# Kernel optimization log

Measured on AMD Instinct MI355X. Metric: run time of the kernel, lower is better.

## Reference

```python
import jax, jax.numpy as jnp
import numpy as np

B, N, IN, HID, H, OUT = 32, 512, 64, 64, 4, 64
NEG_SLOPE = 0.2
NEG_INF = -1e9


def setup_inputs() -> dict:
    key = jax.random.key(0)
    ks = jax.random.split(key, 10)
    s = 0.1
    return {
        "x": jax.random.normal(ks[0], (B, N, IN), jnp.float32),
        "adj": jax.random.randint(ks[1], (B, N, N), 0, 2, jnp.int32),
        "W1": jax.random.normal(ks[2], (IN, H * HID), jnp.float32) * s,
        "a1_src": jax.random.normal(ks[3], (H, HID), jnp.float32) * s,
        "a1_dst": jax.random.normal(ks[4], (H, HID), jnp.float32) * s,
        "b1": jnp.zeros((H * HID,), jnp.float32),
        "W2": jax.random.normal(ks[5], (H * HID, OUT), jnp.float32) * s,
        "a2_src": jax.random.normal(ks[6], (1, OUT), jnp.float32) * s,
        "a2_dst": jax.random.normal(ks[7], (1, OUT), jnp.float32) * s,
        "b2": jnp.zeros((OUT,), jnp.float32),
    }


def _gat_layer(x, mask, W, a_src, a_dst, b, heads, feat):
    # x: [N, Fin]; mask: [N_dst, N_src] bool (edge src->dst), self-loops included
    h = (x @ W).reshape(N, heads, feat)              # [N, H, F]
    e_src = jnp.einsum('nhf,hf->nh', h, a_src)       # [N, H]
    e_dst = jnp.einsum('nhf,hf->nh', h, a_dst)       # [N, H]
    # scores[d, s, h] = leaky_relu(a_dst.x_d + a_src.x_s)
    scores = jax.nn.leaky_relu(e_dst[:, None, :] + e_src[None, :, :], NEG_SLOPE)
    scores = jnp.where(mask[:, :, None], scores, NEG_INF)
    alpha = jax.nn.softmax(scores, axis=1)           # segment-softmax over src neighbors
    out = jnp.einsum('dsh,shf->dhf', alpha, h)       # aggregate messages
    return out.reshape(N, heads * feat) + b


def reference(x, adj, W1, a1_src, a1_dst, b1, W2, a2_src, a2_dst, b2):
    eye = jnp.eye(N, dtype=bool)

    def one_graph(xi, ai):
        # edge i->j when adj[i, j] != 0 (coo row=src, col=dst); add self-loops
        mask = (ai != 0).T | eye                     # [dst, src]
        h1 = jax.nn.elu(_gat_layer(xi, mask, W1, a1_src, a1_dst, b1, H, HID))
        return _gat_layer(h1, mask, W2, a2_src, a2_dst, b2, 1, OUT)

    return jax.vmap(one_graph)(x, adj)               # [B, N, OUT]
```

## Files before the change

### kernel.cpp

```cpp
#include <hip/hip_runtime.h>
#include <cstddef>

#define NN 512
#define NEG_SLOPE 0.2f

typedef __attribute__((ext_vector_type(8))) short short8;
typedef __attribute__((ext_vector_type(16))) float f32x16;

__device__ __forceinline__ unsigned short f2bf(float v) {
  unsigned u = __float_as_uint(v);
  return (unsigned short)((u + 0x7FFFu + ((u >> 16) & 1u)) >> 16);
}

__global__ __launch_bounds__(256) void k_prep(
    const int* __restrict__ adj, const float* __restrict__ x,
    const float* __restrict__ W1, const float* __restrict__ a1s,
    const float* __restrict__ a1d, const float* __restrict__ W2,
    const float* __restrict__ a2s, const float* __restrict__ a2d,
    unsigned* __restrict__ mask, short8* __restrict__ xA,
    short8* __restrict__ W1B, short8* __restrict__ W2B) {
  int blk = blockIdx.x, t = threadIdx.x;
  if (blk < 512) {
    int b = blk >> 4, w = blk & 15;
    const int* base = adj + (size_t)b * NN * NN + (size_t)w * 32 * NN;
#pragma unroll
    for (int half = 0; half < 2; ++half) {
      int d = t + half * 256;
      unsigned wv = 0;
#pragma unroll
      for (int j = 0; j < 32; ++j) {
        unsigned bit = ((base[(size_t)j * NN + d] != 0) || (w * 32 + j == d)) ? 1u : 0u;
        wv |= bit << j;
      }
      mask[((size_t)b * 16 + w) * NN + d] = wv;
    }
  } else if (blk < 1024) {
    int idx = (blk - 512) * 256 + t;
    int u = idx >> 6, lane = idx & 63;
    int b = u >> 6, mt = (u >> 2) & 15, kt = u & 3;
    int node = mt * 32 + (lane & 31);
    int k0 = kt * 16 + ((lane >> 5) << 3);
    const float* xp = x + ((size_t)b * NN + node) * 64 + k0;
    short8 r;
#pragma unroll
    for (int j = 0; j < 8; ++j) r[j] = (short)f2bf(xp[j]);
    xA[idx] = r;
  } else if (blk < 1033) {
    int idx = (blk - 1024) * 256 + t;
    int unit = idx >> 6, lane = idx & 63;
    int nt = unit >> 2, kt = unit & 3;
    int k0 = kt * 16 + ((lane >> 5) << 3);
    short8 r;
    if (nt < 8) {
      int f = nt * 32 + (lane & 31);
#pragma unroll
      for (int j = 0; j < 8; ++j) r[j] = (short)f2bf(W1[(k0 + j) * 256 + f]);
    } else {
      int c = lane & 31;
#pragma unroll
      for (int j = 0; j < 8; ++j) r[j] = 0;
      if (c < 8) {
        int h = c & 3;
        const float* av = ((c < 4) ? a1s : a1d) + h * 64;
#pragma unroll
        for (int j = 0; j < 8; ++j) {
          float s = 0.f;
          for (int f2 = 0; f2 < 64; ++f2)
            s += W1[(k0 + j) * 256 + h * 64 + f2] * av[f2];
          r[j] = (short)f2bf(s);
        }
      }
    }
    W1B[idx] = r;
  } else {
    int idx = (blk - 1033) * 256 + t;
    int unit = idx >> 6, lane = idx & 63;
    int nt = unit >> 4, kt = unit & 15;
    int k0 = kt * 16 + ((lane >> 5) << 3);
    short8 r;
    if (nt < 2) {
      int f = nt * 32 + (lane & 31);
#pragma unroll
      for (int j = 0; j < 8; ++j) r[j] = (short)f2bf(W2[(k0 + j) * 64 + f]);
    } else {
      int c = lane & 31;
#pragma unroll
      for (int j = 0; j < 8; ++j) r[j] = 0;
      if (c < 2) {
        const float* av = (c == 0) ? a2s : a2d;
#pragma unroll
        for (int j = 0; j < 8; ++j) {
          float s = 0.f;
          for (int f2 = 0; f2 < 64; ++f2) s += W2[(k0 + j) * 64 + f2] * av[f2];
          r[j] = (short)f2bf(s);
        }
      }
    }
    W2B[idx] = r;
  }
}

__global__ __launch_bounds__(64) void k_gemm1(const short8* __restrict__ xA,
                                              const short8* __restrict__ W1B,
                                              unsigned short* __restrict__ hb1,
                                              float* __restrict__ e1s,
                                              float* __restrict__ e1d) {
  __shared__ float tile[32 * 33];
  int b = blockIdx.x >> 4, mt = blockIdx.x & 15;
  int lane = threadIdx.x, m = lane & 31, kg = lane >> 5;
  short8 a[4];
#pragma unroll
  for (int kt = 0; kt < 4; ++kt)
    a[kt] = xA[((size_t)(b * 16 + mt) * 4 + kt) * 64 + lane];
  short8* hb8 = (short8*)hb1;
  for (int nt = 0; nt < 9; ++nt) {
    f32x16 acc;
#pragma unroll
    for (int i = 0; i < 16; ++i) acc[i] = 0.f;
#pragma unroll
    for (int kt = 0; kt < 4; ++kt)
      acc = __builtin_amdgcn_mfma_f32_32x32x16_bf16(
          a[kt], W1B[(nt * 4 + kt) * 64 + lane], acc, 0, 0, 0);
    if (nt < 8) {
#pragma unroll
      for (int reg = 0; reg < 16; ++reg) {
        int row = (reg & 3) + 8 * (reg >> 2) + 4 * kg;
        tile[row * 33 + m] = acc[reg];
      }
      __syncthreads();
      int h = nt >> 1, ft = nt & 1;
#pragma unroll
      for (int ktl = 0; ktl < 2; ++ktl) {
        short8 r;
#pragma unroll
        for (int j = 0; j < 8; ++j)
          r[j] = (short)f2bf(tile[(ktl * 16 + kg * 8 + j) * 33 + m]);
        hb8[((((size_t)b * 4 + h) * 32 + mt * 2 + ktl) * 2 + ft) * 64 + lane] = r;
      }
      __syncthreads();
    } else {
      if (m < 8) {
        float* p = ((m < 4) ? e1s : e1d) + ((size_t)b * 4 + (m & 3)) * NN + mt * 32;
#pragma unroll
        for (int reg = 0; reg < 16; ++reg) {
          int row = (reg & 3) + 8 * (reg >> 2) + 4 * kg;
          p[row] = acc[reg];
        }
      }
    }
  }
}

__global__ __launch_bounds__(256) void k_attn1(const unsigned* __restrict__ mask,
                                               const unsigned short* __restrict__ hb1,
                                               const float* __restrict__ e1s,
                                               const float* __restrict__ e1d,
                                               const float* __restrict__ b1,
                                               short8* __restrict__ hA) {
  __shared__ float es[4 * NN];
  __shared__ unsigned mw[16 * 32];
  __shared__ unsigned short ht[32 * 264];
  int b = blockIdx.x >> 4;
  int mt = blockIdx.x & 15;
  int d0 = mt * 32;
  int t = threadIdx.x;
  const float* esrc = e1s + (size_t)b * 4 * NN;
#pragma unroll
  for (int i = 0; i < 8; ++i) es[t + i * 256] = esrc[t + i * 256];
  const unsigned* msrc = mask + (size_t)b * 16 * NN + d0;
  mw[t] = msrc[(t >> 5) * NN + (t & 31)];
  {
    int idx = t + 256;
    mw[idx] = msrc[(idx >> 5) * NN + (idx & 31)];
  }
  __syncthreads();
  int h = t >> 6, lane = t & 63, m = lane & 31, kg = lane >> 5;
  float ed = e1d[((size_t)b * 4 + h) * NN + d0 + m];
  const short8* bfr = (const short8*)hb1 + ((size_t)b * 4 + h) * 32 * 2 * 64;
  f32x16 acc0, acc1;
#pragma unroll
  for (int i = 0; i < 16; ++i) { acc0[i] = 0.f; acc1[i] = 0.f; }
  float l = 0.f;
  for (int kt = 0; kt < 32; ++kt) {
    unsigned wv = mw[(kt >> 1) * 32 + m];
    int shift = (kt & 1) * 16 + kg * 8;
    const float* ep = &es[h * NN + kt * 16 + kg * 8];
    short8 a;
#pragma unroll
    for (int j = 0; j < 8; ++j) {
      float sc = ed + ep[j];
      sc = fmaxf(sc, NEG_SLOPE * sc);
      float pv = __expf(sc);
      pv = ((wv >> (shift + j)) & 1u) ? pv : 0.f;
      l += pv;
      a[j] = (short)f2bf(pv);
    }
    short8 bv0 = bfr[(kt * 2 + 0) * 64 + lane];
    short8 bv1 = bfr[(kt * 2 + 1) * 64 + lane];
    acc0 = __builtin_amdgcn_mfma_f32_32x32x16_bf16(a, bv0, acc0, 0, 0, 0);
    acc1 = __builtin_amdgcn_mfma_f32_32x32x16_bf16(a, bv1, acc1, 0, 0, 0);
  }
  float lf = l + __shfl(l, lane ^ 32, 64);
  float linv = 1.f / lf;
  float bia0 = b1[h * 64 + m];
  float bia1 = b1[h * 64 + 32 + m];
#pragma unroll
  for (int reg = 0; reg < 16; ++reg) {
    int row = (reg & 3) + 8 * (reg >> 2) + 4 * kg;
    float li = __shfl(linv, row, 64);
    float v0 = acc0[reg] * li + bia0;
    v0 = (v0 > 0.f) ? v0 : (__expf(v0) - 1.f);
    float v1 = acc1[reg] * li + bia1;
    v1 = (v1 > 0.f) ? v1 : (__expf(v1) - 1.f);
    ht[row * 264 + h * 64 + m] = f2bf(v0);
    ht[row * 264 + h * 64 + 32 + m] = f2bf(v1);
  }
  __syncthreads();
  int lane2 = t & 63, w = t >> 6;
  int nl = lane2 & 31, kgo = (lane2 >> 5) * 8;
#pragma unroll
  for (int kk = 0; kk < 4; ++kk) {
    int kt = w * 4 + kk;
    short8 av = *(const short8*)&ht[nl * 264 + kt * 16 + kgo];
    hA[((size_t)(b * 16 + mt) * 16 + kt) * 64 + lane2] = av;
  }
}

__global__ __launch_bounds__(64) void k_gemm2(const short8* __restrict__ hA,
                                              const short8* __restrict__ W2B,
                                              unsigned short* __restrict__ hb2,
                                              float* __restrict__ e2s,
                                              float* __restrict__ e2d) {
  __shared__ float tile[32 * 33];
  int b = blockIdx.x >> 4, mt = blockIdx.x & 15;
  int lane = threadIdx.x, m = lane & 31, kg = lane >> 5;
  short8 a[16];
#pragma unroll
  for (int kt = 0; kt < 16; ++kt)
    a[kt] = hA[((size_t)(b * 16 + mt) * 16 + kt) * 64 + lane];
  short8* hb8 = (short8*)hb2;
  for (int nt = 0; nt < 3; ++nt) {
    f32x16 acc;
#pragma unroll
    for (int i = 0; i < 16; ++i) acc[i] = 0.f;
#pragma unroll
    for (int kt = 0; kt < 16; ++kt)
      acc = __builtin_amdgcn_mfma_f32_32x32x16_bf16(
          a[kt], W2B[(nt * 16 + kt) * 64 + lane], acc, 0, 0, 0);
    if (nt < 2) {
#pragma unroll
      for (int reg = 0; reg < 16; ++reg) {
        int row = (reg & 3) + 8 * (reg >> 2) + 4 * kg;
        tile[row * 33 + m] = acc[reg];
      }
      __syncthreads();
#pragma unroll
      for (int ktl = 0; ktl < 2; ++ktl) {
        short8 r;
#pragma unroll
        for (int j = 0; j < 8; ++j)
          r[j] = (short)f2bf(tile[(ktl * 16 + kg * 8 + j) * 33 + m]);
        hb8[(((size_t)b * 32 + mt * 2 + ktl) * 2 + nt) * 64 + lane] = r;
      }
      __syncthreads();
    } else {
      if (m < 2) {
        float* p = ((m == 0) ? e2s : e2d) + (size_t)b * NN + mt * 32;
#pragma unroll
        for (int reg = 0; reg < 16; ++reg) {
          int row = (reg & 3) + 8 * (reg >> 2) + 4 * kg;
          p[row] = acc[reg];
        }
      }
    }
  }
}

__global__ __launch_bounds__(256) void k_attn2(const unsigned* __restrict__ mask,
                                               const unsigned short* __restrict__ hb2,
                                               const float* __restrict__ e2s,
                                               const float* __restrict__ e2d,
                                               const float* __restrict__ b2,
                                               float* __restrict__ out) {
  __shared__ float es[NN];
  __shared__ unsigned mw[16 * 32];
  __shared__ float cred[4][2][16][64];
  __shared__ float lred[4][64];
  __shared__ float linv_s[32];
  int b = blockIdx.x >> 4;
  int d0 = (blockIdx.x & 15) * 32;
  int t = threadIdx.x;
  es[t] = e2s[(size_t)b * NN + t];
  es[t + 256] = e2s[(size_t)b * NN + t + 256];
  const unsigned* msrc = mask + (size_t)b * 16 * NN + d0;
  mw[t] = msrc[(t >> 5) * NN + (t & 31)];
  {
    int idx = t + 256;
    mw[idx] = msrc[(idx >> 5) * NN + (idx & 31)];
  }
  __syncthreads();
  int w = t >> 6, lane = t & 63, m = lane & 31, kg = lane >> 5;
  float ed = e2d[(size_t)b * NN + d0 + m];
  const short8* bfr = (const short8*)hb2 + (size_t)b * 32 * 2 * 64;
  f32x16 acc0, acc1;
#pragma unroll
  for (int i = 0; i < 16; ++i) { acc0[i] = 0.f; acc1[i] = 0.f; }
  float l = 0.f;
#pragma unroll
  for (int kk = 0; kk < 8; ++kk) {
    int kt = w * 8 + kk;
    unsigned wv = mw[(kt >> 1) * 32 + m];
    int shift = (kt & 1) * 16 + kg * 8;
    const float* ep = &es[kt * 16 + kg * 8];
    short8 a;
#pragma unroll
    for (int j = 0; j < 8; ++j) {
      float sc = ed + ep[j];
      sc = fmaxf(sc, NEG_SLOPE * sc);
      float pv = __expf(sc);
      pv = ((wv >> (shift + j)) & 1u) ? pv : 0.f;
      l += pv;
      a[j] = (short)f2bf(pv);
    }
    short8 bv0 = bfr[(kt * 2 + 0) * 64 + lane];
    short8 bv1 = bfr[(kt * 2 + 1) * 64 + lane];
    acc0 = __builtin_amdgcn_mfma_f32_32x32x16_bf16(a, bv0, acc0, 0, 0, 0);
    acc1 = __builtin_amdgcn_mfma_f32_32x32x16_bf16(a, bv1, acc1, 0, 0, 0);
  }
  lred[w][lane] = l;
#pragma unroll
  for (int reg = 0; reg < 16; ++reg) {
    cred[w][0][reg][lane] = acc0[reg];
    cred[w][1][reg][lane] = acc1[reg];
  }
  __syncthreads();
  if (t < 32) {
    float s = 0.f;
#pragma unroll
    for (int i = 0; i < 4; ++i) s += lred[i][t] + lred[i][t + 32];
    linv_s[t] = 1.f / s;
  }
  __syncthreads();
#pragma unroll
  for (int i = 0; i < 8; ++i) {
    int pos = t + i * 256;
    int nt = pos >> 10;
    int rem = pos & 1023;
    int reg = rem >> 6;
    int ln = rem & 63;
    float v = cred[0][nt][reg][ln] + cred[1][nt][reg][ln] +
              cred[2][nt][reg][ln] + cred[3][nt][reg][ln];
    int row = (reg & 3) + 8 * (reg >> 2) + 4 * (ln >> 5);
    int col = nt * 32 + (ln & 31);
    out[((size_t)b * NN + d0 + row) * 64 + col] = v * linv_s[row] + b2[col];
  }
}

extern "C" void kernel_launch(void* const* d_in, const int* in_sizes, int n_in,
                              void* d_out, int out_size, void* d_ws, size_t ws_size,
                              hipStream_t stream) {
  const float* x = (const float*)d_in[0];
  const int* adj = (const int*)d_in[1];
  const float* W1 = (const float*)d_in[2];
  const float* a1s = (const float*)d_in[3];
  const float* a1d = (const float*)d_in[4];
  const float* b1 = (const float*)d_in[5];
  const float* W2 = (const float*)d_in[6];
  const float* a2s = (const float*)d_in[7];
  const float* a2d = (const float*)d_in[8];
  const float* b2 = (const float*)d_in[9];
  float* out = (float*)d_out;

  char* w = (char*)d_ws;
  unsigned* mask = (unsigned*)w;
  short8* xA = (short8*)(w + (1u << 20));
  short8* W1B = (short8*)(w + (3u << 20));
  short8* W2B = (short8*)(w + (3u << 20) + (64u << 10));
  unsigned short* hb1 = (unsigned short*)(w + (4u << 20));
  float* e1s = (float*)(w + (12u << 20));
  float* e1d = (float*)(w + (12u << 20) + (256u << 10));
  short8* hA = (short8*)(w + (13u << 20));
  unsigned short* hb2 = (unsigned short*)(w + (21u << 20));
  float* e2s = (float*)(w + (23u << 20));
  float* e2d = (float*)(w + (23u << 20) + (64u << 10));

  hipLaunchKernelGGL(k_prep, dim3(1045), dim3(256), 0, stream, adj, x, W1, a1s,
                     a1d, W2, a2s, a2d, mask, xA, W1B, W2B);
  hipLaunchKernelGGL(k_gemm1, dim3(512), dim3(64), 0, stream, xA, W1B, hb1,
                     e1s, e1d);
  hipLaunchKernelGGL(k_attn1, dim3(512), dim3(256), 0, stream, mask, hb1, e1s,
                     e1d, b1, hA);
  hipLaunchKernelGGL(k_gemm2, dim3(512), dim3(64), 0, stream, hA, W2B, hb2,
                     e2s, e2d);
  hipLaunchKernelGGL(k_attn2, dim3(512), dim3(256), 0, stream, mask, hb2, e2s,
                     e2d, b2, out);
}
```

Measured before the change: 147.4 us.

## Fuse layer-2 GEMM into attention-1 kernel and convert x inline in GEMM1

Folds k_gemm2 into the layer-1 attention kernel, so the layer-1 output tile in LDS feeds layer-2 MFMAs directly instead of going through the hA global buffer and a separate launch. GEMM1 now reads fp32 x and converts to bf16 itself, which removes the xA prep pass. The W·a projections in k_prep are computed once per (k, column) in LDS instead of redundantly per lane. Block indices are remapped so the 32 graphs are spread across blocks, which may change L2 locality. The cost is more LDS per block in the fused kernel and only 3 of 4 waves doing the GEMM2 work.

```diff
diff --git a/kernel.cpp b/kernel.cpp
--- a/kernel.cpp
+++ b/kernel.cpp
@@ -13,11 +13,10 @@
 }
 
 __global__ __launch_bounds__(256) void k_prep(
-    const int* __restrict__ adj, const float* __restrict__ x,
-    const float* __restrict__ W1, const float* __restrict__ a1s,
-    const float* __restrict__ a1d, const float* __restrict__ W2,
-    const float* __restrict__ a2s, const float* __restrict__ a2d,
-    unsigned* __restrict__ mask, short8* __restrict__ xA,
+    const int* __restrict__ adj, const float* __restrict__ W1,
+    const float* __restrict__ a1s, const float* __restrict__ a1d,
+    const float* __restrict__ W2, const float* __restrict__ a2s,
+    const float* __restrict__ a2d, unsigned* __restrict__ mask,
     short8* __restrict__ W1B, short8* __restrict__ W2B) {
   int blk = blockIdx.x, t = threadIdx.x;
   if (blk < 512) {
@@ -34,89 +33,97 @@
       }
       mask[((size_t)b * 16 + w) * NN + d] = wv;
     }
-  } else if (blk < 1024) {
-    int idx = (blk - 512) * 256 + t;
-    int u = idx >> 6, lane = idx & 63;
-    int b = u >> 6, mt = (u >> 2) & 15, kt = u & 3;
-    int node = mt * 32 + (lane & 31);
-    int k0 = kt * 16 + ((lane >> 5) << 3);
-    const float* xp = x + ((size_t)b * NN + node) * 64 + k0;
-    short8 r;
-#pragma unroll
-    for (int j = 0; j < 8; ++j) r[j] = (short)f2bf(xp[j]);
-    xA[idx] = r;
-  } else if (blk < 1033) {
-    int idx = (blk - 1024) * 256 + t;
-    int unit = idx >> 6, lane = idx & 63;
-    int nt = unit >> 2, kt = unit & 3;
-    int k0 = kt * 16 + ((lane >> 5) << 3);
-    short8 r;
-    if (nt < 8) {
+  } else if (blk < 521) {
+    int blk2 = blk - 512;
+    if (blk2 < 8) {
+      int idx = blk2 * 256 + t;
+      int unit = idx >> 6, lane = idx & 63;
+      int nt = unit >> 2, kt = unit & 3;
       int f = nt * 32 + (lane & 31);
+      int k0 = kt * 16 + ((lane >> 5) << 3);
+      short8 r;
 #pragma unroll
       for (int j = 0; j < 8; ++j) r[j] = (short)f2bf(W1[(k0 + j) * 256 + f]);
+      W1B[idx] = r;
     } else {
-      int c = lane & 31;
-#pragma unroll
-      for (int j = 0; j < 8; ++j) r[j] = 0;
-      if (c < 8) {
-        int h = c & 3;
+      __shared__ float wa1[64][8];
+#pragma unroll
+      for (int rep = 0; rep < 2; ++rep) {
+        int id = t + rep * 256;
+        int k = id >> 3, c = id & 7, h = c & 3;
         const float* av = ((c < 4) ? a1s : a1d) + h * 64;
-#pragma unroll
-        for (int j = 0; j < 8; ++j) {
-          float s = 0.f;
-          for (int f2 = 0; f2 < 64; ++f2)
-            s += W1[(k0 + j) * 256 + h * 64 + f2] * av[f2];
-          r[j] = (short)f2bf(s);
-        }
-      }
-    }
-    W1B[idx] = r;
+        float s = 0.f;
+        for (int f2 = 0; f2 < 64; ++f2) s += W1[k * 256 + h * 64 + f2] * av[f2];
+        wa1[k][c] = s;
+      }
+      __syncthreads();
+      int kt = t >> 6, lane = t & 63, col = lane & 31, kg = lane >> 5;
+      short8 r;
+#pragma unroll
+      for (int j = 0; j < 8; ++j)
+        r[j] = (col < 8) ? (short)f2bf(wa1[kt * 16 + kg * 8 + j][col]) : (short)0;
+      W1B[2048 + t] = r;
+    }
   } else {
-    int idx = (blk - 1033) * 256 + t;
-    int unit = idx >> 6, lane = idx & 63;
-    int nt = unit >> 4, kt = unit & 15;
-    int k0 = kt * 16 + ((lane >> 5) << 3);
-    short8 r;
-    if (nt < 2) {
+    int blk3 = blk - 521;
+    if (blk3 < 8) {
+      int idx = blk3 * 256 + t;
+      int unit = idx >> 6, lane = idx & 63;
+      int nt = unit >> 4, kt = unit & 15;
       int f = nt * 32 + (lane & 31);
+      int k0 = kt * 16 + ((lane >> 5) << 3);
+      short8 r;
 #pragma unroll
       for (int j = 0; j < 8; ++j) r[j] = (short)f2bf(W2[(k0 + j) * 64 + f]);
+      W2B[idx] = r;
     } else {
-      int c = lane & 31;
-#pragma unroll
-      for (int j = 0; j < 8; ++j) r[j] = 0;
-      if (c < 2) {
+      __shared__ float wa2[64][2];
+      int kbase = (blk3 - 8) * 64;
+      if (t < 128) {
+        int k = t >> 1, c = t & 1;
         const float* av = (c == 0) ? a2s : a2d;
-#pragma unroll
-        for (int j = 0; j < 8; ++j) {
-          float s = 0.f;
-          for (int f2 = 0; f2 < 64; ++f2) s += W2[(k0 + j) * 64 + f2] * av[f2];
-          r[j] = (short)f2bf(s);
-        }
-      }
-    }
-    W2B[idx] = r;
-  }
-}
-
-__global__ __launch_bounds__(64) void k_gemm1(const short8* __restrict__ xA,
+        float s = 0.f;
+        for (int f2 = 0; f2 < 64; ++f2) s += W2[(kbase + k) * 64 + f2] * av[f2];
+        wa2[k][c] = s;
+      }
+      __syncthreads();
+      int ktl = t >> 6, lane = t & 63, col = lane & 31, kg = lane >> 5;
+      short8 r;
+#pragma unroll
+      for (int j = 0; j < 8; ++j)
+        r[j] = (col < 2) ? (short)f2bf(wa2[ktl * 16 + kg * 8 + j][col]) : (short)0;
+      W2B[2048 + (blk3 - 8) * 256 + t] = r;
+    }
+  }
+}
+
+__global__ __launch_bounds__(64) void k_gemm1(const float* __restrict__ x,
                                               const short8* __restrict__ W1B,
                                               unsigned short* __restrict__ hb1,
                                               float* __restrict__ e1s,
                                               float* __restrict__ e1d) {
   __shared__ float tile[32 * 33];
-  int b = blockIdx.x >> 4, mt = blockIdx.x & 15;
+  int i = blockIdx.x;
+  int b = (i & 7) * 4 + ((i >> 3) & 3), mt = i >> 5;
   int lane = threadIdx.x, m = lane & 31, kg = lane >> 5;
+  const float* xrow = x + ((size_t)b * NN + mt * 32 + m) * 64 + kg * 8;
   short8 a[4];
 #pragma unroll
-  for (int kt = 0; kt < 4; ++kt)
-    a[kt] = xA[((size_t)(b * 16 + mt) * 4 + kt) * 64 + lane];
+  for (int kt = 0; kt < 4; ++kt) {
+    float4 v0 = *(const float4*)(xrow + kt * 16);
+    float4 v1 = *(const float4*)(xrow + kt * 16 + 4);
+    short8 r;
+    r[0] = (short)f2bf(v0.x); r[1] = (short)f2bf(v0.y);
+    r[2] = (short)f2bf(v0.z); r[3] = (short)f2bf(v0.w);
+    r[4] = (short)f2bf(v1.x); r[5] = (short)f2bf(v1.y);
+    r[6] = (short)f2bf(v1.z); r[7] = (short)f2bf(v1.w);
+    a[kt] = r;
+  }
   short8* hb8 = (short8*)hb1;
   for (int nt = 0; nt < 9; ++nt) {
     f32x16 acc;
 #pragma unroll
-    for (int i = 0; i < 16; ++i) acc[i] = 0.f;
+    for (int q = 0; q < 16; ++q) acc[q] = 0.f;
 #pragma unroll
     for (int kt = 0; kt < 4; ++kt)
       acc = __builtin_amdgcn_mfma_f32_32x32x16_bf16(
@@ -151,22 +158,26 @@
   }
 }
 
-__global__ __launch_bounds__(256) void k_attn1(const unsigned* __restrict__ mask,
-                                               const unsigned short* __restrict__ hb1,
-                                               const float* __restrict__ e1s,
-                                               const float* __restrict__ e1d,
-                                               const float* __restrict__ b1,
-                                               short8* __restrict__ hA) {
+__global__ __launch_bounds__(256) void k_attn1g2(const unsigned* __restrict__ mask,
+                                                 const unsigned short* __restrict__ hb1,
+                                                 const float* __restrict__ e1s,
+                                                 const float* __restrict__ e1d,
+                                                 const float* __restrict__ b1,
+                                                 const short8* __restrict__ W2B,
+                                                 unsigned short* __restrict__ hb2,
+                                                 float* __restrict__ e2s,
+                                                 float* __restrict__ e2d) {
   __shared__ float es[4 * NN];
   __shared__ unsigned mw[16 * 32];
   __shared__ unsigned short ht[32 * 264];
-  int b = blockIdx.x >> 4;
-  int mt = blockIdx.x & 15;
+  __shared__ float tile2[2 * 32 * 33];
+  int i = blockIdx.x;
+  int b = (i & 7) * 4 + ((i >> 3) & 3), mt = i >> 5;
   int d0 = mt * 32;
   int t = threadIdx.x;
   const float* esrc = e1s + (size_t)b * 4 * NN;
 #pragma unroll
-  for (int i = 0; i < 8; ++i) es[t + i * 256] = esrc[t + i * 256];
+  for (int q = 0; q < 8; ++q) es[t + q * 256] = esrc[t + q * 256];
   const unsigned* msrc = mask + (size_t)b * 16 * NN + d0;
   mw[t] = msrc[(t >> 5) * NN + (t & 31)];
   {
@@ -179,7 +190,7 @@
   const short8* bfr = (const short8*)hb1 + ((size_t)b * 4 + h) * 32 * 2 * 64;
   f32x16 acc0, acc1;
 #pragma unroll
-  for (int i = 0; i < 16; ++i) { acc0[i] = 0.f; acc1[i] = 0.f; }
+  for (int q = 0; q < 16; ++q) { acc0[q] = 0.f; acc1[q] = 0.f; }
   float l = 0.f;
   for (int kt = 0; kt < 32; ++kt) {
     unsigned wv = mw[(kt >> 1) * 32 + m];
@@ -216,59 +227,40 @@
     ht[row * 264 + h * 64 + 32 + m] = f2bf(v1);
   }
   __syncthreads();
-  int lane2 = t & 63, w = t >> 6;
-  int nl = lane2 & 31, kgo = (lane2 >> 5) * 8;
-#pragma unroll
-  for (int kk = 0; kk < 4; ++kk) {
-    int kt = w * 4 + kk;
-    short8 av = *(const short8*)&ht[nl * 264 + kt * 16 + kgo];
-    hA[((size_t)(b * 16 + mt) * 16 + kt) * 64 + lane2] = av;
-  }
-}
-
-__global__ __launch_bounds__(64) void k_gemm2(const short8* __restrict__ hA,
-                                              const short8* __restrict__ W2B,
-                                              unsigned short* __restrict__ hb2,
-                                              float* __restrict__ e2s,
-                                              float* __restrict__ e2d) {
-  __shared__ float tile[32 * 33];
-  int b = blockIdx.x >> 4, mt = blockIdx.x & 15;
-  int lane = threadIdx.x, m = lane & 31, kg = lane >> 5;
-  short8 a[16];
-#pragma unroll
-  for (int kt = 0; kt < 16; ++kt)
-    a[kt] = hA[((size_t)(b * 16 + mt) * 16 + kt) * 64 + lane];
-  short8* hb8 = (short8*)hb2;
-  for (int nt = 0; nt < 3; ++nt) {
+  int w2 = t >> 6, lane2 = t & 63, m2 = lane2 & 31, kg2 = lane2 >> 5;
+  if (w2 < 3) {
+    int nt = w2;
     f32x16 acc;
 #pragma unroll
-    for (int i = 0; i < 16; ++i) acc[i] = 0.f;
-#pragma unroll
-    for (int kt = 0; kt < 16; ++kt)
+    for (int q = 0; q < 16; ++q) acc[q] = 0.f;
+#pragma unroll
+    for (int kt = 0; kt < 16; ++kt) {
+      short8 av = *(const short8*)&ht[m2 * 264 + kt * 16 + kg2 * 8];
       acc = __builtin_amdgcn_mfma_f32_32x32x16_bf16(
-          a[kt], W2B[(nt * 16 + kt) * 64 + lane], acc, 0, 0, 0);
+          av, W2B[(nt * 16 + kt) * 64 + lane2], acc, 0, 0, 0);
+    }
     if (nt < 2) {
+      float* tw = tile2 + nt * (32 * 33);
 #pragma unroll
       for (int reg = 0; reg < 16; ++reg) {
-        int row = (reg & 3) + 8 * (reg >> 2) + 4 * kg;
-        tile[row * 33 + m] = acc[reg];
-      }
-      __syncthreads();
+        int row = (reg & 3) + 8 * (reg >> 2) + 4 * kg2;
+        tw[row * 33 + m2] = acc[reg];
+      }
+      short8* hb8 = (short8*)hb2;
 #pragma unroll
       for (int ktl = 0; ktl < 2; ++ktl) {
         short8 r;
 #pragma unroll
         for (int j = 0; j < 8; ++j)
-          r[j] = (short)f2bf(tile[(ktl * 16 + kg * 8 + j) * 33 + m]);
-        hb8[(((size_t)b * 32 + mt * 2 + ktl) * 2 + nt) * 64 + lane] = r;
-      }
-      __syncthreads();
+          r[j] = (short)f2bf(tw[(ktl * 16 + kg2 * 8 + j) * 33 + m2]);
+        hb8[(((size_t)b * 32 + mt * 2 + ktl) * 2 + nt) * 64 + lane2] = r;
+      }
     } else {
-      if (m < 2) {
-        float* p = ((m == 0) ? e2s : e2d) + (size_t)b * NN + mt * 32;
+      if (m2 < 2) {
+        float* p = ((m2 == 0) ? e2s : e2d) + (size_t)b * NN + mt * 32;
 #pragma unroll
         for (int reg = 0; reg < 16; ++reg) {
-          int row = (reg & 3) + 8 * (reg >> 2) + 4 * kg;
+          int row = (reg & 3) + 8 * (reg >> 2) + 4 * kg2;
           p[row] = acc[reg];
         }
       }
@@ -287,8 +279,9 @@
   __shared__ float cred[4][2][16][64];
   __shared__ float lred[4][64];
   __shared__ float linv_s[32];
-  int b = blockIdx.x >> 4;
-  int d0 = (blockIdx.x & 15) * 32;
+  int i = blockIdx.x;
+  int b = (i & 7) * 4 + ((i >> 3) & 3);
+  int d0 = (i >> 5) * 32;
   int t = threadIdx.x;
   es[t] = e2s[(size_t)b * NN + t];
   es[t + 256] = e2s[(size_t)b * NN + t + 256];
@@ -304,7 +297,7 @@
   const short8* bfr = (const short8*)hb2 + (size_t)b * 32 * 2 * 64;
   f32x16 acc0, acc1;
 #pragma unroll
-  for (int i = 0; i < 16; ++i) { acc0[i] = 0.f; acc1[i] = 0.f; }
+  for (int q = 0; q < 16; ++q) { acc0[q] = 0.f; acc1[q] = 0.f; }
   float l = 0.f;
 #pragma unroll
   for (int kk = 0; kk < 8; ++kk) {
@@ -337,13 +330,13 @@
   if (t < 32) {
     float s = 0.f;
 #pragma unroll
-    for (int i = 0; i < 4; ++i) s += lred[i][t] + lred[i][t + 32];
+    for (int q = 0; q < 4; ++q) s += lred[q][t] + lred[q][t + 32];
     linv_s[t] = 1.f / s;
   }
   __syncthreads();
 #pragma unroll
-  for (int i = 0; i < 8; ++i) {
-    int pos = t + i * 256;
+  for (int q = 0; q < 8; ++q) {
+    int pos = t + q * 256;
     int nt = pos >> 10;
     int rem = pos & 1023;
     int reg = rem >> 6;
@@ -373,25 +366,21 @@
 
   char* w = (char*)d_ws;
   unsigned* mask = (unsigned*)w;
-  short8* xA = (short8*)(w + (1u << 20));
   short8* W1B = (short8*)(w + (3u << 20));
   short8* W2B = (short8*)(w + (3u << 20) + (64u << 10));
   unsigned short* hb1 = (unsigned short*)(w + (4u << 20));
   float* e1s = (float*)(w + (12u << 20));
   float* e1d = (float*)(w + (12u << 20) + (256u << 10));
-  short8* hA = (short8*)(w + (13u << 20));
   unsigned short* hb2 = (unsigned short*)(w + (21u << 20));
   float* e2s = (float*)(w + (23u << 20));
   float* e2d = (float*)(w + (23u << 20) + (64u << 10));
 
-  hipLaunchKernelGGL(k_prep, dim3(1045), dim3(256), 0, stream, adj, x, W1, a1s,
-                     a1d, W2, a2s, a2d, mask, xA, W1B, W2B);
-  hipLaunchKernelGGL(k_gemm1, dim3(512), dim3(64), 0, stream, xA, W1B, hb1,
+  hipLaunchKernelGGL(k_prep, dim3(533), dim3(256), 0, stream, adj, W1, a1s,
+                     a1d, W2, a2s, a2d, mask, W1B, W2B);
+  hipLaunchKernelGGL(k_gemm1, dim3(512), dim3(64), 0, stream, x, W1B, hb1,
                      e1s, e1d);
-  hipLaunchKernelGGL(k_attn1, dim3(512), dim3(256), 0, stream, mask, hb1, e1s,
-                     e1d, b1, hA);
-  hipLaunchKernelGGL(k_gemm2, dim3(512), dim3(64), 0, stream, hA, W2B, hb2,
-                     e2s, e2d);
+  hipLaunchKernelGGL(k_attn1g2, dim3(512), dim3(256), 0, stream, mask, hb1,
+                     e1s, e1d, b1, W2B, hb2, e2s, e2d);
   hipLaunchKernelGGL(k_attn2, dim3(512), dim3(256), 0, stream, mask, hb2, e2s,
                      e2d, b2, out);
 }
```

New measurement: 133.3 us. 1.11x faster.
